# Optimization experiments

Hardware: AMD Instinct MI355X
Metric: run time of the kernel (lower is better)

Reference implementation:

```python
import jax, jax.numpy as jnp
import numpy as np

B, N, D = 1, 4301, 768          # batch, tokens (4200 patch + 1 cls + 100 det), dim
H, HD = 12, 64                  # heads, head_dim (all_head_dim = 768)
NDET = 100                      # det tokens at the end of the sequence
EPS = 1e-5                      # torch LayerNorm default eps
SCALE = HD ** -0.5


def setup_inputs() -> dict:
    key = jax.random.key(0)
    ks = jax.random.split(key, 10)
    w = lambda k: jax.random.normal(k, (D, D), dtype=jnp.float32) * 0.02
    return {
        "x": jax.random.normal(ks[0], (B, N, D), dtype=jnp.float32),
        "wq_p": w(ks[1]), "wk_p": w(ks[2]), "wv_p": w(ks[3]),
        "wq_d": w(ks[4]), "wk_d": w(ks[5]), "wv_d": w(ks[6]),
        "bq_p": jnp.zeros((D,), jnp.float32), "bv_p": jnp.zeros((D,), jnp.float32),
        "bq_d": jnp.zeros((D,), jnp.float32), "bv_d": jnp.zeros((D,), jnp.float32),
        "ln_g": jnp.ones((D,), jnp.float32), "ln_b": jnp.zeros((D,), jnp.float32),
        "wo_p": w(ks[7]), "bo_p": jnp.zeros((D,), jnp.float32),
        "wo_d": w(ks[8]), "bo_d": jnp.zeros((D,), jnp.float32),
    }


def reference(x, wq_p, wk_p, wv_p, wq_d, wk_d, wv_d,
              bq_p, bv_p, bq_d, bv_d, ln_g, ln_b,
              wo_p, bo_p, wo_d, bo_d):
    xp = x[:, :-NDET, :]                       # [B, N-100, D] patch (+cls) tokens
    xd = x[:, -NDET:, :]                       # [B, 100, D]   det tokens
    # separate patch/det QKV projections (subln=True path; k has no bias)
    q = jnp.concatenate([xp @ wq_p.T + bq_p, xd @ wq_d.T + bq_d], axis=1)
    k = jnp.concatenate([xp @ wk_p.T,        xd @ wk_d.T],        axis=1)
    v = jnp.concatenate([xp @ wv_p.T + bv_p, xd @ wv_d.T + bv_d], axis=1)
    split = lambda t: t.reshape(B, N, H, HD).transpose(0, 2, 1, 3)  # [B,H,N,HD]
    q, k, v = split(q) * SCALE, split(k), split(v)
    # unfused attention (memory_efficient_attention_pytorch, attn_mask=None)
    attn = jax.nn.softmax(jnp.einsum("bhqd,bhkd->bhqk", q, k), axis=-1)
    o = jnp.einsum("bhqk,bhkd->bhqd", attn, v)
    o = o.transpose(0, 2, 1, 3).reshape(B, N, D)
    # inner_attn_ln (LayerNorm over all_head_dim)
    mu = o.mean(-1, keepdims=True)
    var = ((o - mu) ** 2).mean(-1, keepdims=True)
    o = (o - mu) * jax.lax.rsqrt(var + EPS) * ln_g + ln_b
    # separate patch/det output projections
    out = jnp.concatenate([o[:, :-NDET, :] @ wo_p.T + bo_p,
                           o[:, -NDET:, :] @ wo_d.T + bo_d], axis=1)
    return out
```

## Files before the change

kernel.cpp:

```cpp
#include <hip/hip_runtime.h>
#include <hip/hip_bf16.h>

#define NT 4301
#define NP 4201
#define NDET 100
#define DMODEL 768
#define NHEAD 12
#define HD 64
#define LN_EPS 1e-5f
#define LOG2E 1.4426950408889634f
#define QSCALE (0.125f * LOG2E)
#define NTP 4352
#define NCHUNK 68
#define FRAGSZ 512
#define CHUNKSZ 4096

typedef __hip_bfloat16 bf16;
typedef __attribute__((ext_vector_type(4))) float f32x4;
typedef __attribute__((ext_vector_type(8))) short frag8;
typedef __attribute__((ext_vector_type(2))) unsigned int u32x2;

static __device__ __forceinline__ void permlane32_swap(unsigned& a, unsigned& b) {
#if __has_builtin(__builtin_amdgcn_permlane32_swap)
    u32x2 r = __builtin_amdgcn_permlane32_swap(a, b, false, false);
    a = r[0]; b = r[1];
#else
    asm("v_permlane32_swap_b32 %0, %1" : "+v"(a), "+v"(b));
#endif
}
static __device__ __forceinline__ void permlane16_swap(unsigned& a, unsigned& b) {
#if __has_builtin(__builtin_amdgcn_permlane16_swap)
    u32x2 r = __builtin_amdgcn_permlane16_swap(a, b, false, false);
    a = r[0]; b = r[1];
#else
    asm("v_permlane16_swap_b32 %0, %1" : "+v"(a), "+v"(b));
#endif
}

static __device__ __forceinline__ float fast_exp2(float x) {
#if __has_builtin(__builtin_amdgcn_exp2f)
    return __builtin_amdgcn_exp2f(x);
#else
    return __builtin_exp2f(x);
#endif
}

static __device__ __forceinline__ unsigned pack_bf16_tr(float a, float b) {
    return __builtin_amdgcn_perm(__builtin_bit_cast(unsigned, b),
                                 __builtin_bit_cast(unsigned, a), 0x07060302u);
}

static __device__ __forceinline__ void gload16(const bf16* g, bf16* l) {
    __builtin_amdgcn_global_load_lds(
        (const __attribute__((address_space(1))) void*)g,
        (__attribute__((address_space(3))) void*)l, 16, 0, 0);
}

__global__ __launch_bounds__(256) void cast_all_kernel(
    const float* __restrict__ x,
    const float* __restrict__ w0, const float* __restrict__ w1,
    const float* __restrict__ w2, const float* __restrict__ w3,
    const float* __restrict__ w4, const float* __restrict__ w5,
    const float* __restrict__ w6, const float* __restrict__ w7,
    bf16* __restrict__ dst, int nx, int nw, int total) {
    int i4 = (blockIdx.x * 256 + threadIdx.x) * 4;
    if (i4 >= total) return;
    const float* s;
    int off;
    if (i4 < nx) {
        s = x; off = i4;
    } else {
        int r = i4 - nx;
        int w = r / nw;
        off = r - w * nw;
        s = w0;
        if (w == 1) s = w1; else if (w == 2) s = w2; else if (w == 3) s = w3;
        else if (w == 4) s = w4; else if (w == 5) s = w5;
        else if (w == 6) s = w6; else if (w == 7) s = w7;
    }
    float4 v = *(const float4*)(s + off);
    bf16 o[4] = {__float2bfloat16(v.x), __float2bfloat16(v.y),
                 __float2bfloat16(v.z), __float2bfloat16(v.w)};
    *(ushort4*)(dst + i4) = *(ushort4*)o;
}

__global__ __launch_bounds__(256, 4) void qkv_kernel(
    const bf16* __restrict__ xb, const bf16* __restrict__ wbase,
    const float* __restrict__ bq_p, const float* __restrict__ bq_d,
    const float* __restrict__ bv_p, const float* __restrict__ bv_d,
    bf16* __restrict__ Qb, bf16* __restrict__ Ksw, bf16* __restrict__ Vsw) {
    __shared__ bf16 As[64][32];
    __shared__ bf16 Bs[192][32];

    const int tid = threadIdx.x;
    const int wave = tid >> 6, lane = tid & 63;
    const int quad = lane >> 4, l16 = lane & 15;
    const int bx = blockIdx.x;
    const int h = blockIdx.y;
    const int is_det = bx >= 66;
    const int row0 = is_det ? NP + (bx - 66) * 64 : bx * 64;
    const int Mlim = is_det ? NT : NP;
    const int col0 = h * 64;
    const size_t nw = (size_t)DMODEL * DMODEL;
    const bf16* W = wbase + (is_det ? 3 * nw : 0);

    const f32x4 z4 = {0.f, 0.f, 0.f, 0.f};
    f32x4 acc[4][3];
#pragma unroll
    for (int r4 = 0; r4 < 4; ++r4)
#pragma unroll
        for (int f = 0; f < 3; ++f) acc[r4][f] = z4;

    const int srow = tid >> 2;
    const int scol8 = (tid & 3) * 8;
    int a_r = row0 + srow;
    if (a_r >= Mlim) a_r = Mlim - 1;
    const bf16* ap = xb + (size_t)a_r * DMODEL + scol8;
    const bf16* bp = W + (size_t)(col0 + srow) * DMODEL + scol8;

    uint4 areg  = *(const uint4*)(ap);
    uint4 breg0 = *(const uint4*)(bp);
    uint4 breg1 = *(const uint4*)(bp + nw);
    uint4 breg2 = *(const uint4*)(bp + 2 * nw);

    for (int k0 = 0; k0 < DMODEL; k0 += 32) {
        __syncthreads();
        *(uint4*)(&As[srow][scol8]) = areg;
        *(uint4*)(&Bs[srow][scol8]) = breg0;
        *(uint4*)(&Bs[64 + srow][scol8]) = breg1;
        *(uint4*)(&Bs[128 + srow][scol8]) = breg2;
        if (k0 + 32 < DMODEL) {
            areg  = *(const uint4*)(ap + k0 + 32);
            breg0 = *(const uint4*)(bp + k0 + 32);
            breg1 = *(const uint4*)(bp + nw + k0 + 32);
            breg2 = *(const uint4*)(bp + 2 * nw + k0 + 32);
        }
        __asm__ volatile("s_waitcnt lgkmcnt(0)" ::: "memory");
        __builtin_amdgcn_s_barrier();
        __asm__ volatile("" ::: "memory");
        frag8 af[4], bfr[3];
#pragma unroll
        for (int r4 = 0; r4 < 4; ++r4)
            af[r4] = *(const frag8*)(&As[r4 * 16 + l16][quad * 8]);
#pragma unroll
        for (int f = 0; f < 3; ++f)
            bfr[f] = *(const frag8*)(&Bs[wave * 48 + f * 16 + l16][quad * 8]);
#pragma unroll
        for (int r4 = 0; r4 < 4; ++r4)
#pragma unroll
            for (int f = 0; f < 3; ++f)
                acc[r4][f] = __builtin_amdgcn_mfma_f32_16x16x32_bf16(af[r4], bfr[f], acc[r4][f], 0, 0, 0);
        __asm__ volatile("" ::: "memory");
    }

#pragma unroll
    for (int f = 0; f < 3; ++f) {
        const int oc = 3 * wave + f;
        const int opi = oc >> 2;
        const int cin = (oc & 3) * 16 + l16;
        const int c = col0 + cin;
        float bv = 0.f, scale = 1.f;
        if (opi == 0) { bv = (is_det ? bq_d : bq_p)[c]; scale = QSCALE; }
        else if (opi == 2) { bv = (is_det ? bv_d : bv_p)[c]; }
#pragma unroll
        for (int r4 = 0; r4 < 4; ++r4) {
#pragma unroll
            for (int j = 0; j < 4; ++j) {
                const int r = row0 + r4 * 16 + quad * 4 + j;
                if (r >= Mlim) continue;
                const bf16 val = __float2bfloat16((acc[r4][f][j] + bv) * scale);
                if (opi == 0) {
                    Qb[(size_t)r * DMODEL + c] = val;
                } else if (opi == 1) {
                    const int cc = r >> 6, tf = (r >> 4) & 3, ln = r & 15;
                    const int s = cin >> 5, qd = (cin >> 3) & 3, je = cin & 7;
                    Ksw[((size_t)(h * NCHUNK + cc) * 8 + tf * 2 + s) * FRAGSZ +
                        (qd * 16 + ln) * 8 + je] = val;
                } else {
                    const int t = cin >> 4, le = cin & 15;
                    const int cc = r >> 6, rr = r & 63;
                    const int sv = rr >> 5, qv = (rr >> 3) & 3, je = rr & 7;
                    Vsw[((size_t)(h * NCHUNK + cc) * 8 + t * 2 + sv) * FRAGSZ +
                        (qv * 16 + le) * 8 + je] = val;
                }
            }
        }
    }
}

__global__ __launch_bounds__(256, 4) void attn_kernel(
    const bf16* __restrict__ Q, const bf16* __restrict__ Ksw,
    const bf16* __restrict__ Vsw, float* __restrict__ O_part,
    float* __restrict__ l_part, int cpb) {
    __shared__ bf16 KV[2][16][FRAGSZ];

    const int tid = threadIdx.x;
    const int wave = tid >> 6, lane = tid & 63;
    const int quad = lane >> 4, l16 = lane & 15;

    int bx, h, z;
    {
        const int id = blockIdx.x;
        const int nblk = gridDim.x;
        const int per = nblk >> 3;
        if ((nblk & 7) == 0 && per % 34 == 0) {
            const int ppx = per / 34;
            const int q = id >> 3;
            const int pair = (id & 7) * ppx + q / 34;
            bx = q % 34;
            h = pair % NHEAD; z = pair / NHEAD;
        } else {
            bx = id % 34; h = (id / 34) % NHEAD; z = id / (34 * NHEAD);
        }
    }
    const int qbase = bx * 128;
    const int hoff = h * HD;
    const int c0 = z * cpb, c1 = c0 + cpb;

    frag8 ones;
#pragma unroll
    for (int j = 0; j < 8; ++j) ones[j] = (short)0x3F80;

    frag8 qf[2][2];
#pragma unroll
    for (int g = 0; g < 2; ++g) {
        int qr = qbase + wave * 32 + g * 16 + l16;
        if (qr >= NT) qr = NT - 1;
#pragma unroll
        for (int s = 0; s < 2; ++s)
            qf[g][s] = *(const frag8*)(Q + (size_t)qr * DMODEL + hoff + s * 32 + quad * 8);
    }

    const bf16* kb0 = Ksw + (size_t)h * NCHUNK * CHUNKSZ + lane * 8;
    const bf16* vb0 = Vsw + (size_t)h * NCHUNK * CHUNKSZ + lane * 8;
    const bf16* sb = (wave < 2) ? kb0 : vb0;
    const int foff = (wave & 1) * 4;
    const int fbase = 4 * wave;

    const f32x4 z4 = {0.f, 0.f, 0.f, 0.f};
    f32x4 accO[2][4], accL[2];
#pragma unroll
    for (int g = 0; g < 2; ++g) {
        accL[g] = z4;
#pragma unroll
        for (int t = 0; t < 4; ++t) accO[g][t] = z4;
    }

    {
        const bf16* s = sb + (size_t)c0 * CHUNKSZ + foff * FRAGSZ;
#pragma unroll
        for (int i = 0; i < 4; ++i)
            gload16(s + i * FRAGSZ, &KV[0][fbase + i][0]);
    }
    __asm__ volatile("s_waitcnt vmcnt(0)" ::: "memory");
    __builtin_amdgcn_s_barrier();
    __asm__ volatile("" ::: "memory");

    int p = 0;
    for (int c = c0; c < c1; ++c) {
        if (c + 1 < c1) {
            const bf16* s = sb + (size_t)(c + 1) * CHUNKSZ + foff * FRAGSZ;
#pragma unroll
            for (int i = 0; i < 4; ++i)
                gload16(s + i * FRAGSZ, &KV[p ^ 1][fbase + i][0]);
        }

        f32x4 S[2][4];
#pragma unroll
        for (int t = 0; t < 4; ++t) {
            const frag8 k0 = *(const frag8*)(&KV[p][t * 2 + 0][lane * 8]);
            const frag8 k1 = *(const frag8*)(&KV[p][t * 2 + 1][lane * 8]);
#pragma unroll
            for (int g = 0; g < 2; ++g) {
                f32x4 s0 = __builtin_amdgcn_mfma_f32_16x16x32_bf16(k0, qf[g][0], z4, 0, 0, 0);
                S[g][t]  = __builtin_amdgcn_mfma_f32_16x16x32_bf16(k1, qf[g][1], s0, 0, 0, 0);
            }
        }
        if (c == NCHUNK - 1) {
            const int kb = c * 64 + quad * 4;
#pragma unroll
            for (int t = 0; t < 4; ++t)
#pragma unroll
                for (int j = 0; j < 4; ++j)
                    if (kb + t * 16 + j >= NT) {
                        S[0][t][j] = -1e30f;
                        S[1][t][j] = -1e30f;
                    }
        }

        frag8 pf[2][2];
#pragma unroll
        for (int g = 0; g < 2; ++g) {
            unsigned lo[4], hi[4];
#pragma unroll
            for (int t = 0; t < 4; ++t) {
                lo[t] = pack_bf16_tr(fast_exp2(S[g][t][0]), fast_exp2(S[g][t][1]));
                hi[t] = pack_bf16_tr(fast_exp2(S[g][t][2]), fast_exp2(S[g][t][3]));
            }
#pragma unroll
            for (int s = 0; s < 2; ++s) {
                unsigned A = lo[2 * s], B = hi[2 * s];
                unsigned C = lo[2 * s + 1], D = hi[2 * s + 1];
                permlane32_swap(A, C);
                permlane32_swap(B, D);
                permlane16_swap(A, C);
                permlane16_swap(B, D);
                union { unsigned u[4]; frag8 f; } pu;
                pu.u[0] = A; pu.u[1] = B; pu.u[2] = C; pu.u[3] = D;
                pf[g][s] = pu.f;
                accL[g] = __builtin_amdgcn_mfma_f32_16x16x32_bf16(pf[g][s], ones, accL[g], 0, 0, 0);
            }
        }

#pragma unroll
        for (int s = 0; s < 2; ++s)
#pragma unroll
            for (int t = 0; t < 4; ++t) {
                const frag8 v = *(const frag8*)(&KV[p][8 + t * 2 + s][lane * 8]);
#pragma unroll
                for (int g = 0; g < 2; ++g)
                    accO[g][t] = __builtin_amdgcn_mfma_f32_16x16x32_bf16(pf[g][s], v, accO[g][t], 0, 0, 0);
            }

        __asm__ volatile("s_waitcnt vmcnt(0)" ::: "memory");
        __builtin_amdgcn_s_barrier();
        __asm__ volatile("" ::: "memory");
        p ^= 1;
    }

    float* Op = O_part + (size_t)z * NT * DMODEL;
#pragma unroll
    for (int g = 0; g < 2; ++g)
#pragma unroll
        for (int j = 0; j < 4; ++j) {
            const int r = qbase + wave * 32 + g * 16 + quad * 4 + j;
            if (r < NT) {
#pragma unroll
                for (int t = 0; t < 4; ++t)
                    Op[(size_t)r * DMODEL + hoff + t * 16 + l16] = accO[g][t][j];
                if (l16 == 0)
                    l_part[((size_t)z * NHEAD + h) * NTP + r] = accL[g][j];
            }
        }
}

__global__ __launch_bounds__(192) void reduce_ln_kernel(
    const float* __restrict__ O_part, const float* __restrict__ l_part,
    const float* __restrict__ g, const float* __restrict__ b,
    bf16* __restrict__ out, int nsplit) {
    const int n = blockIdx.x;
    const int tid = threadIdx.x;
    const int d0 = tid * 4;
    const int hh = d0 >> 6;

    float4 o = make_float4(0.f, 0.f, 0.f, 0.f);
    float lv = 0.f;
    for (int s = 0; s < nsplit; ++s) {
        float4 v = *(const float4*)(O_part + ((size_t)s * NT + n) * DMODEL + d0);
        o.x += v.x; o.y += v.y; o.z += v.z; o.w += v.w;
        lv += l_part[((size_t)s * NHEAD + hh) * NTP + n];
    }
    const float inv_l = 1.0f / lv;
    float vals[4] = {o.x * inv_l, o.y * inv_l, o.z * inv_l, o.w * inv_l};

    float s = vals[0] + vals[1] + vals[2] + vals[3];
    float s2 = vals[0] * vals[0] + vals[1] * vals[1] + vals[2] * vals[2] + vals[3] * vals[3];
#pragma unroll
    for (int off = 1; off < 64; off <<= 1) {
        s += __shfl_xor(s, off);
        s2 += __shfl_xor(s2, off);
    }
    __shared__ float ss[3], ss2[3];
    const int wave = tid >> 6, lane = tid & 63;
    if (lane == 0) { ss[wave] = s; ss2[wave] = s2; }
    __syncthreads();
    s = ss[0] + ss[1] + ss[2];
    s2 = ss2[0] + ss2[1] + ss2[2];
    const float mu = s * (1.0f / 768.0f);
    float var = s2 * (1.0f / 768.0f) - mu * mu;
    const float inv = rsqrtf(var + LN_EPS);

    unsigned short pk[4];
#pragma unroll
    for (int i = 0; i < 4; ++i) {
        const int d = d0 + i;
        const float v = (vals[i] - mu) * inv * g[d] + b[d];
        bf16 bb = __float2bfloat16(v);
        pk[i] = *(unsigned short*)&bb;
    }
    *(ushort4*)(out + (size_t)n * DMODEL + d0) = *(ushort4*)pk;
}

__global__ __launch_bounds__(256, 2) void out_kernel(
    const bf16* __restrict__ Lb, const bf16* __restrict__ wo,
    const float* __restrict__ bo_p, const float* __restrict__ bo_d,
    float* __restrict__ out) {
    __shared__ bf16 As[128][32];
    __shared__ bf16 Bs[64][32];

    const int tid = threadIdx.x;
    const int wave = tid >> 6, lane = tid & 63;
    const int quad = lane >> 4, l16 = lane & 15;
    const int bx = blockIdx.x;
    const int is_det = bx >= 33;
    const int row0 = is_det ? NP : bx * 128;
    const int Mlim = is_det ? NT : NP;
    const int col0 = blockIdx.y * 64;
    const size_t nw = (size_t)DMODEL * DMODEL;
    const bf16* B = wo + (is_det ? nw : 0);
    const float* bias = is_det ? bo_d : bo_p;

    const f32x4 z4 = {0.f, 0.f, 0.f, 0.f};
    f32x4 acc[2][4];
#pragma unroll
    for (int gg = 0; gg < 2; ++gg)
#pragma unroll
        for (int t = 0; t < 4; ++t) acc[gg][t] = z4;

    const int arow = tid >> 1;
    const int acol = (tid & 1) * 16;
    int a_r = row0 + arow;
    if (a_r >= Mlim) a_r = Mlim - 1;
    const bf16* ap = Lb + (size_t)a_r * DMODEL + acol;
    const int brow = tid >> 2;
    const int bcol = (tid & 3) * 8;
    const bf16* bp = B + (size_t)(col0 + brow) * DMODEL + bcol;

    uint4 areg0 = *(const uint4*)(ap);
    uint4 areg1 = *(const uint4*)(ap + 8);
    uint4 breg  = *(const uint4*)(bp);

    for (int k0 = 0; k0 < DMODEL; k0 += 32) {
        __syncthreads();
        *(uint4*)(&As[arow][acol]) = areg0;
        *(uint4*)(&As[arow][acol + 8]) = areg1;
        *(uint4*)(&Bs[brow][bcol]) = breg;
        if (k0 + 32 < DMODEL) {
            areg0 = *(const uint4*)(ap + k0 + 32);
            areg1 = *(const uint4*)(ap + k0 + 40);
            breg  = *(const uint4*)(bp + k0 + 32);
        }
        __asm__ volatile("s_waitcnt lgkmcnt(0)" ::: "memory");
        __builtin_amdgcn_s_barrier();
        __asm__ volatile("" ::: "memory");
        frag8 af[2], bfq[4];
#pragma unroll
        for (int gg = 0; gg < 2; ++gg)
            af[gg] = *(const frag8*)(&As[wave * 32 + gg * 16 + l16][quad * 8]);
#pragma unroll
        for (int t = 0; t < 4; ++t)
            bfq[t] = *(const frag8*)(&Bs[t * 16 + l16][quad * 8]);
#pragma unroll
        for (int gg = 0; gg < 2; ++gg)
#pragma unroll
            for (int t = 0; t < 4; ++t)
                acc[gg][t] = __builtin_amdgcn_mfma_f32_16x16x32_bf16(af[gg], bfq[t], acc[gg][t], 0, 0, 0);
        __asm__ volatile("" ::: "memory");
    }

#pragma unroll
    for (int gg = 0; gg < 2; ++gg) {
        const int rbase = row0 + wave * 32 + gg * 16 + quad * 4;
#pragma unroll
        for (int t = 0; t < 4; ++t) {
            const int c = col0 + t * 16 + l16;
            const float bv = bias[c];
#pragma unroll
            for (int j = 0; j < 4; ++j) {
                const int r = rbase + j;
                if (r < Mlim) out[(size_t)r * DMODEL + c] = acc[gg][t][j] + bv;
            }
        }
    }
}

extern "C" void kernel_launch(void* const* d_in, const int* in_sizes, int n_in,
                              void* d_out, int out_size, void* d_ws, size_t ws_size,
                              hipStream_t stream) {
    const float* x    = (const float*)d_in[0];
    const float* wq_p = (const float*)d_in[1];
    const float* wk_p = (const float*)d_in[2];
    const float* wv_p = (const float*)d_in[3];
    const float* wq_d = (const float*)d_in[4];
    const float* wk_d = (const float*)d_in[5];
    const float* wv_d = (const float*)d_in[6];
    const float* bq_p = (const float*)d_in[7];
    const float* bv_p = (const float*)d_in[8];
    const float* bq_d = (const float*)d_in[9];
    const float* bv_d = (const float*)d_in[10];
    const float* ln_g = (const float*)d_in[11];
    const float* ln_b = (const float*)d_in[12];
    const float* wo_p = (const float*)d_in[13];
    const float* bo_p = (const float*)d_in[14];
    const float* wo_d = (const float*)d_in[15];
    const float* bo_d = (const float*)d_in[16];
    float* out = (float*)d_out;

    const size_t nx  = (size_t)NT * DMODEL;
    const size_t nsw = (size_t)NHEAD * NCHUNK * CHUNKSZ;
    const size_t nw  = (size_t)DMODEL * DMODEL;

    char* ws = (char*)d_ws;
    bf16* xb   = (bf16*)ws; ws += nx * 2;
    bf16* wqkv = (bf16*)ws; ws += 6 * nw * 2;
    bf16* wob  = (bf16*)ws; ws += 2 * nw * 2;
    bf16* Qb   = (bf16*)ws; ws += nx * 2;
    bf16* Ksw  = (bf16*)ws; ws += nsw * 2;
    bf16* Vsw  = (bf16*)ws; ws += nsw * 2;
    const size_t fixed = (size_t)(ws - (char*)d_ws);

    const size_t per_split = nx * 4 + (size_t)NHEAD * NTP * 4;
    int nsplit = 1;
    if (ws_size >= fixed + 4 * per_split) nsplit = 4;
    else if (ws_size >= fixed + 2 * per_split) nsplit = 2;
    const int cpb = NCHUNK / nsplit;

    float* O_part = (float*)ws;
    float* l_part = (float*)(ws + (size_t)nsplit * nx * 4);
    bf16* Lb = xb;

    const int total = (int)(nx + 8 * nw);
    cast_all_kernel<<<dim3((total / 4 + 255) / 256), dim3(256), 0, stream>>>(
        x, wq_p, wk_p, wv_p, wq_d, wk_d, wv_d, wo_p, wo_d, xb, (int)nx, (int)nw, total);

    qkv_kernel<<<dim3(68, 12), dim3(256), 0, stream>>>(
        xb, wqkv, bq_p, bq_d, bv_p, bv_d, Qb, Ksw, Vsw);

    attn_kernel<<<dim3(34 * NHEAD * nsplit), dim3(256), 0, stream>>>(
        Qb, Ksw, Vsw, O_part, l_part, cpb);

    reduce_ln_kernel<<<dim3(NT), dim3(192), 0, stream>>>(
        O_part, l_part, ln_g, ln_b, Lb, nsplit);

    out_kernel<<<dim3(34, 12), dim3(256), 0, stream>>>(Lb, wob, bo_p, bo_d, out);
}
```

Measured before the change: 232.7 us.

## Double-buffer QKV GEMM LDS tiles with direct global-to-LDS loads

Switches the QKV projection kernel from register-staged loads to direct global-to-LDS loads (gload16) into double-buffered shared tiles, so the next K-slice's fetch overlaps the MFMA work on the current one. This drops one barrier per iteration and removes the register round-trip. It doubles LDS use per block. It also raises the out_kernel occupancy hint from 2 to 4 blocks per CU, which may constrain registers.

```diff
diff --git a/kernel.cpp b/kernel.cpp
--- a/kernel.cpp
+++ b/kernel.cpp
@@ -89,8 +89,8 @@
     const float* __restrict__ bq_p, const float* __restrict__ bq_d,
     const float* __restrict__ bv_p, const float* __restrict__ bv_d,
     bf16* __restrict__ Qb, bf16* __restrict__ Ksw, bf16* __restrict__ Vsw) {
-    __shared__ bf16 As[64][32];
-    __shared__ bf16 Bs[192][32];
+    __shared__ bf16 As[2][64][32];
+    __shared__ bf16 Bs[2][192][32];
 
     const int tid = threadIdx.x;
     const int wave = tid >> 6, lane = tid & 63;
@@ -118,39 +118,44 @@
     const bf16* ap = xb + (size_t)a_r * DMODEL + scol8;
     const bf16* bp = W + (size_t)(col0 + srow) * DMODEL + scol8;
 
-    uint4 areg  = *(const uint4*)(ap);
-    uint4 breg0 = *(const uint4*)(bp);
-    uint4 breg1 = *(const uint4*)(bp + nw);
-    uint4 breg2 = *(const uint4*)(bp + 2 * nw);
-
+    bf16* asb[2] = {&As[0][0][0] + wave * 512, &As[1][0][0] + wave * 512};
+    bf16* bsb[2] = {&Bs[0][0][0] + wave * 512, &Bs[1][0][0] + wave * 512};
+
+    {
+        gload16(ap, asb[0]);
+        gload16(bp, bsb[0]);
+        gload16(bp + nw, bsb[0] + 2048);
+        gload16(bp + 2 * nw, bsb[0] + 4096);
+    }
+    __asm__ volatile("s_waitcnt vmcnt(0)" ::: "memory");
+    __builtin_amdgcn_s_barrier();
+    __asm__ volatile("" ::: "memory");
+
+    int p = 0;
     for (int k0 = 0; k0 < DMODEL; k0 += 32) {
-        __syncthreads();
-        *(uint4*)(&As[srow][scol8]) = areg;
-        *(uint4*)(&Bs[srow][scol8]) = breg0;
-        *(uint4*)(&Bs[64 + srow][scol8]) = breg1;
-        *(uint4*)(&Bs[128 + srow][scol8]) = breg2;
         if (k0 + 32 < DMODEL) {
-            areg  = *(const uint4*)(ap + k0 + 32);
-            breg0 = *(const uint4*)(bp + k0 + 32);
-            breg1 = *(const uint4*)(bp + nw + k0 + 32);
-            breg2 = *(const uint4*)(bp + 2 * nw + k0 + 32);
-        }
-        __asm__ volatile("s_waitcnt lgkmcnt(0)" ::: "memory");
+            const int kn = k0 + 32;
+            gload16(ap + kn, asb[p ^ 1]);
+            gload16(bp + kn, bsb[p ^ 1]);
+            gload16(bp + nw + kn, bsb[p ^ 1] + 2048);
+            gload16(bp + 2 * nw + kn, bsb[p ^ 1] + 4096);
+        }
+        frag8 af[4], bfr[3];
+#pragma unroll
+        for (int r4 = 0; r4 < 4; ++r4)
+            af[r4] = *(const frag8*)(&As[p][r4 * 16 + l16][quad * 8]);
+#pragma unroll
+        for (int f = 0; f < 3; ++f)
+            bfr[f] = *(const frag8*)(&Bs[p][wave * 48 + f * 16 + l16][quad * 8]);
+#pragma unroll
+        for (int r4 = 0; r4 < 4; ++r4)
+#pragma unroll
+            for (int f = 0; f < 3; ++f)
+                acc[r4][f] = __builtin_amdgcn_mfma_f32_16x16x32_bf16(af[r4], bfr[f], acc[r4][f], 0, 0, 0);
+        __asm__ volatile("s_waitcnt vmcnt(0)" ::: "memory");
         __builtin_amdgcn_s_barrier();
         __asm__ volatile("" ::: "memory");
-        frag8 af[4], bfr[3];
-#pragma unroll
-        for (int r4 = 0; r4 < 4; ++r4)
-            af[r4] = *(const frag8*)(&As[r4 * 16 + l16][quad * 8]);
-#pragma unroll
-        for (int f = 0; f < 3; ++f)
-            bfr[f] = *(const frag8*)(&Bs[wave * 48 + f * 16 + l16][quad * 8]);
-#pragma unroll
-        for (int r4 = 0; r4 < 4; ++r4)
-#pragma unroll
-            for (int f = 0; f < 3; ++f)
-                acc[r4][f] = __builtin_amdgcn_mfma_f32_16x16x32_bf16(af[r4], bfr[f], acc[r4][f], 0, 0, 0);
-        __asm__ volatile("" ::: "memory");
+        p ^= 1;
     }
 
 #pragma unroll
@@ -391,7 +396,7 @@
     *(ushort4*)(out + (size_t)n * DMODEL + d0) = *(ushort4*)pk;
 }
 
-__global__ __launch_bounds__(256, 2) void out_kernel(
+__global__ __launch_bounds__(256, 4) void out_kernel(
     const bf16* __restrict__ Lb, const bf16* __restrict__ wo,
     const float* __restrict__ bo_p, const float* __restrict__ bo_d,
     float* __restrict__ out) {
```

Result: no change. 229.9 us (-1.2%).
